# Optimization experiments

Measured on AMD Instinct MI355X. Metric: run time of the kernel, lower is better.

Reference implementation:

```python
import jax, jax.numpy as jnp
import numpy as np

D_MODEL = 1024
N_HEADS = 16
HEAD_DIM = D_MODEL // N_HEADS


def setup_inputs() -> dict:
    key = jax.random.key(0)
    k1, k2, k3 = jax.random.split(key, 3)
    x = jax.random.normal(k1, (8, 1024, D_MODEL), dtype=jnp.float32)
    qkv_w = jax.random.normal(k2, (3 * D_MODEL, D_MODEL), dtype=jnp.float32) * 0.02
    qkv_b = jnp.zeros((3 * D_MODEL,), dtype=jnp.float32)
    proj_w = jax.random.normal(k3, (D_MODEL, D_MODEL), dtype=jnp.float32) * 0.02
    proj_b = jnp.zeros((D_MODEL,), dtype=jnp.float32)
    return {"x": x, "qkv_w": qkv_w, "qkv_b": qkv_b, "proj_w": proj_w, "proj_b": proj_b}


def reference(x, qkv_w, qkv_b, proj_w, proj_b):
    B, N, C = x.shape
    H, Dh = N_HEADS, HEAD_DIM
    # fused QKV projection (torch Linear: x @ W^T + b)
    qkv = x @ qkv_w.T + qkv_b                      # [B, N, 3C]
    qkv = qkv.reshape(B, N, 3, H, Dh).transpose(2, 0, 3, 1, 4)  # [3, B, H, N, Dh]
    q, k, v = qkv[0], qkv[1], qkv[2]
    scale = Dh ** -0.5
    attn = jnp.einsum("bhnd,bhmd->bhnm", q, k) * scale  # [B, H, N, N]
    attn = jax.nn.softmax(attn, axis=-1)
    out = jnp.einsum("bhnm,bhmd->bhnd", attn, v)        # [B, H, N, Dh]
    out = out.transpose(0, 2, 1, 3).reshape(B, N, C)
    return out @ proj_w.T + proj_b
```

## Files before the change

### kernel.cpp

```cpp
#include <hip/hip_runtime.h>
#include <hip/hip_bf16.h>
#include <stdint.h>

#define D_MODEL 1024
#define NHEADS  16
#define HDIM    64
#define SEQ     1024
#define BATCH   8

typedef __bf16 bf16;
typedef bf16  bf16x8 __attribute__((ext_vector_type(8)));
typedef float f32x4  __attribute__((ext_vector_type(4)));
typedef uint32_t u32;

#define VMCNT4   asm volatile("s_waitcnt vmcnt(4)" ::: "memory")
#define VMCNT0   asm volatile("s_waitcnt vmcnt(0)" ::: "memory")
#define LGKMCNT0 asm volatile("s_waitcnt lgkmcnt(0)" ::: "memory")
#define SBAR     __builtin_amdgcn_s_barrier()
#define SCHEDB   __builtin_amdgcn_sched_barrier(0)

__device__ __forceinline__ int swzi(int row, int col) {
    return (row << 6) + (col ^ ((row & 7) << 3));
}

__device__ __forceinline__ void gload_lds16(const bf16* g, bf16* l) {
    __builtin_amdgcn_global_load_lds(
        (const __attribute__((address_space(1))) void*)g,
        (__attribute__((address_space(3))) void*)l, 16, 0, 0);
}

__global__ void cvt3_kernel(const float* __restrict__ x,  bf16* __restrict__ ox, int nx,
                            const float* __restrict__ w1, bf16* __restrict__ o1, int n1,
                            const float* __restrict__ w2, bf16* __restrict__ o2, int n2) {
    int i = (blockIdx.x * 256 + threadIdx.x) * 8;
    const float* src; bf16* dst;
    if (i < nx)           { src = x  + i;            dst = ox + i; }
    else if (i < nx + n1) { src = w1 + (i - nx);     dst = o1 + (i - nx); }
    else if (i < nx + n1 + n2) { src = w2 + (i - nx - n1); dst = o2 + (i - nx - n1); }
    else return;
    float4 a = *reinterpret_cast<const float4*>(src);
    float4 b = *reinterpret_cast<const float4*>(src + 4);
    union { bf16 h[8]; uint4 u; } pk;
    pk.h[0] = (bf16)a.x; pk.h[1] = (bf16)a.y; pk.h[2] = (bf16)a.z; pk.h[3] = (bf16)a.w;
    pk.h[4] = (bf16)b.x; pk.h[5] = (bf16)b.y; pk.h[6] = (bf16)b.z; pk.h[7] = (bf16)b.w;
    *reinterpret_cast<uint4*>(dst) = pk.u;
}

__global__ __launch_bounds__(512, 1)
void qkv_gemm8(const bf16* __restrict__ X, const bf16* __restrict__ W,
               const float* __restrict__ bias,
               bf16* __restrict__ q_ws, bf16* __restrict__ k_ws, bf16* __restrict__ vt_ws)
{
    __shared__ __align__(16) bf16 lds[2][2][2][128 * 64];
    const int K = 1024;
    int bid = blockIdx.x;
    int wg  = (bid & 7) * 48 + (bid >> 3);
    int bm = wg / 12, bn = wg % 12;
    int m0 = bm * 256, n0 = bn * 256;
    int tid = threadIdx.x, lane = tid & 63, wid = tid >> 6;
    int wr = wid >> 2, wc = wid & 3;
    int g = lane >> 4, q = lane & 15;
    int bh_half = wc >> 1;
    int brow0   = (wc & 1) * 64;

    const bf16* srcA[2][2]; const bf16* srcB[2][2]; int dstoff[2];
#pragma unroll
    for (int c = 0; c < 2; ++c) {
        int ch = tid + c * 512;
        int r  = ch >> 3;
        int jg = (ch & 7) ^ (r & 7);
        dstoff[c]  = ch * 8;
        srcA[0][c] = X + (size_t)(m0 + r)       * K + jg * 8;
        srcA[1][c] = X + (size_t)(m0 + 128 + r) * K + jg * 8;
        srcB[0][c] = W + (size_t)(n0 + r)       * K + jg * 8;
        srcB[1][c] = W + (size_t)(n0 + 128 + r) * K + jg * 8;
    }

    f32x4 acc[8][4];
#pragma unroll
    for (int i = 0; i < 8; ++i)
#pragma unroll
        for (int j = 0; j < 4; ++j) acc[i][j] = (f32x4){0.f, 0.f, 0.f, 0.f};

#pragma unroll
    for (int h = 0; h < 2; ++h)
#pragma unroll
        for (int c = 0; c < 2; ++c) { gload_lds16(srcA[h][c], &lds[0][0][h][dstoff[c]]); srcA[h][c] += 64; }
#pragma unroll
    for (int h = 0; h < 2; ++h)
#pragma unroll
        for (int c = 0; c < 2; ++c) { gload_lds16(srcB[h][c], &lds[0][1][h][dstoff[c]]); srcB[h][c] += 64; }

    bf16x8 afr[4][2], bfr[2][2][2];

    for (int t = 0; t < 16; ++t) {
        int p = t & 1, np = p ^ 1;
        bf16* Ah = lds[p][0][wr];
        bf16* Bh = lds[p][1][bh_half];

        if (t < 15) {
#pragma unroll
            for (int h = 0; h < 2; ++h)
#pragma unroll
                for (int c = 0; c < 2; ++c) { gload_lds16(srcA[h][c], &lds[np][0][h][dstoff[c]]); srcA[h][c] += 64; }
            VMCNT4;
        } else {
            VMCNT0;
        }
        SBAR;
#pragma unroll
        for (int m = 0; m < 4; ++m)
#pragma unroll
            for (int kk = 0; kk < 2; ++kk)
                afr[m][kk] = *reinterpret_cast<const bf16x8*>(Ah + swzi(m * 16 + q, kk * 32 + g * 8));
#pragma unroll
        for (int nh = 0; nh < 2; ++nh)
#pragma unroll
            for (int n = 0; n < 2; ++n)
#pragma unroll
                for (int kk = 0; kk < 2; ++kk)
                    bfr[nh][n][kk] = *reinterpret_cast<const bf16x8*>(
                        Bh + swzi(brow0 + (nh * 2 + n) * 16 + q, kk * 32 + g * 8));
        LGKMCNT0; SCHEDB;
        __builtin_amdgcn_s_setprio(1);
#pragma unroll
        for (int m = 0; m < 4; ++m)
#pragma unroll
            for (int n = 0; n < 2; ++n)
#pragma unroll
                for (int kk = 0; kk < 2; ++kk)
                    acc[m][n] = __builtin_amdgcn_mfma_f32_16x16x32_bf16(afr[m][kk], bfr[0][n][kk], acc[m][n], 0, 0, 0);
        __builtin_amdgcn_s_setprio(0);
        SBAR;

        if (t < 15) {
#pragma unroll
            for (int h = 0; h < 2; ++h)
#pragma unroll
                for (int c = 0; c < 2; ++c) { gload_lds16(srcB[h][c], &lds[np][1][h][dstoff[c]]); srcB[h][c] += 64; }
        }
        SCHEDB;
        __builtin_amdgcn_s_setprio(1);
#pragma unroll
        for (int m = 0; m < 4; ++m)
#pragma unroll
            for (int n = 0; n < 2; ++n)
#pragma unroll
                for (int kk = 0; kk < 2; ++kk)
                    acc[m][2 + n] = __builtin_amdgcn_mfma_f32_16x16x32_bf16(afr[m][kk], bfr[1][n][kk], acc[m][2 + n], 0, 0, 0);
        __builtin_amdgcn_s_setprio(0);
        SBAR;

#pragma unroll
        for (int m = 0; m < 4; ++m)
#pragma unroll
            for (int kk = 0; kk < 2; ++kk)
                afr[m][kk] = *reinterpret_cast<const bf16x8*>(Ah + swzi(64 + m * 16 + q, kk * 32 + g * 8));
        LGKMCNT0; SCHEDB;
        __builtin_amdgcn_s_setprio(1);
#pragma unroll
        for (int m = 0; m < 4; ++m)
#pragma unroll
            for (int n = 0; n < 2; ++n)
#pragma unroll
                for (int kk = 0; kk < 2; ++kk)
                    acc[4 + m][n] = __builtin_amdgcn_mfma_f32_16x16x32_bf16(afr[m][kk], bfr[0][n][kk], acc[4 + m][n], 0, 0, 0);
        __builtin_amdgcn_s_setprio(0);
        SBAR;

        SCHEDB;
        __builtin_amdgcn_s_setprio(1);
#pragma unroll
        for (int m = 0; m < 4; ++m)
#pragma unroll
            for (int n = 0; n < 2; ++n)
#pragma unroll
                for (int kk = 0; kk < 2; ++kk)
                    acc[4 + m][2 + n] = __builtin_amdgcn_mfma_f32_16x16x32_bf16(afr[m][kk], bfr[1][n][kk], acc[4 + m][2 + n], 0, 0, 0);
        __builtin_amdgcn_s_setprio(0);
        SBAR;
    }

#pragma unroll
    for (int i = 0; i < 8; ++i) {
        int mbase = m0 + wr * 128 + i * 16 + g * 4;
        int b = mbase >> 10, nrow0 = mbase & 1023;
#pragma unroll
        for (int j = 0; j < 4; ++j) {
            int col = n0 + wc * 64 + j * 16 + q;
            int which = col >> 10, rem = col & 1023;
            int h = rem >> 6, d = rem & 63;
            float bi = bias[col];
            int bh = b * NHEADS + h;
            if (which == 2) {
                union { bf16 h4[4]; uint2 u; } vp;
#pragma unroll
                for (int r = 0; r < 4; ++r) vp.h4[r] = (bf16)(acc[i][j][r] + bi);
                *reinterpret_cast<uint2*>(vt_ws + ((size_t)bh * HDIM + d) * SEQ + nrow0) = vp.u;
            } else {
                bf16* dst = (which == 0) ? q_ws : k_ws;
                float scl = (which == 0) ? 0.125f : 1.0f;
#pragma unroll
                for (int r = 0; r < 4; ++r) {
                    float v = (acc[i][j][r] + bi) * scl;
                    dst[((size_t)bh * SEQ + nrow0 + r) * HDIM + d] = (bf16)v;
                }
            }
        }
    }
}

__device__ __forceinline__ void gemm_tile_acc(
    const bf16* __restrict__ A, const bf16* __restrict__ B, int K,
    int m0, int n0, bf16* As, bf16* Bs,
    f32x4 acc[4][4], int wr, int wc, int lane, int tid)
{
    for (int kt = 0; kt < K; kt += 64) {
        __syncthreads();
#pragma unroll
        for (int c = 0; c < 4; ++c) {
            int chunk = tid + c * 256;
            int r   = chunk >> 3;
            int j   = chunk & 7;
            int jg  = j ^ (r & 7);
            gload_lds16(A + (size_t)(m0 + r) * K + kt + jg * 8, As + chunk * 8);
            gload_lds16(B + (size_t)(n0 + r) * K + kt + jg * 8, Bs + chunk * 8);
        }
        __syncthreads();
#pragma unroll
        for (int kk = 0; kk < 2; ++kk) {
            bf16x8 af[4], bfr[4];
#pragma unroll
            for (int t = 0; t < 4; ++t) {
                af[t]  = *reinterpret_cast<const bf16x8*>(As + swzi(wr * 64 + t * 16 + (lane & 15), kk * 32 + ((lane >> 4) << 3)));
                bfr[t] = *reinterpret_cast<const bf16x8*>(Bs + swzi(wc * 64 + t * 16 + (lane & 15), kk * 32 + ((lane >> 4) << 3)));
            }
#pragma unroll
            for (int i = 0; i < 4; ++i)
#pragma unroll
                for (int j2 = 0; j2 < 4; ++j2)
                    acc[i][j2] = __builtin_amdgcn_mfma_f32_16x16x32_bf16(af[i], bfr[j2], acc[i][j2], 0, 0, 0);
        }
    }
}

__global__ __launch_bounds__(256)
void proj_gemm(const bf16* __restrict__ Ao, const bf16* __restrict__ W,
               const float* __restrict__ bias, float* __restrict__ out)
{
    __shared__ __align__(16) bf16 As[128 * 64];
    __shared__ __align__(16) bf16 Bs[128 * 64];
    const int NB = 1024 / 128;
    int bm = blockIdx.x / NB, bn = blockIdx.x % NB;
    int m0 = bm * 128, n0 = bn * 128;
    int tid = threadIdx.x, lane = tid & 63, w = tid >> 6;
    int wr = w >> 1, wc = w & 1;
    f32x4 acc[4][4];
#pragma unroll
    for (int i = 0; i < 4; ++i)
#pragma unroll
        for (int j = 0; j < 4; ++j) acc[i][j] = (f32x4){0.f, 0.f, 0.f, 0.f};

    gemm_tile_acc(Ao, W, 1024, m0, n0, As, Bs, acc, wr, wc, lane, tid);

#pragma unroll
    for (int i = 0; i < 4; ++i) {
        int mbase = m0 + wr * 64 + i * 16 + ((lane >> 4) << 2);
#pragma unroll
        for (int j = 0; j < 4; ++j) {
            int col = n0 + wc * 64 + j * 16 + (lane & 15);
            float bi = bias[col];
#pragma unroll
            for (int r = 0; r < 4; ++r)
                out[(size_t)(mbase + r) * D_MODEL + col] = acc[i][j][r] + bi;
        }
    }
}

__global__ __launch_bounds__(256)
void attn_kernel(const bf16* __restrict__ Q, const bf16* __restrict__ K,
                 const bf16* __restrict__ Vt, bf16* __restrict__ AO)
{
    __shared__ __align__(16) bf16 kl[128 * 64];
    __shared__ __align__(16) bf16 vl[64 * 128];
    int bh = blockIdx.x & 127;
    int qt = blockIdx.x >> 7;
    int tid = threadIdx.x, lane = tid & 63, w = tid >> 6;
    int g = lane >> 4, q = lane & 15;
    const bf16* Qb  = Q  + (size_t)bh * SEQ * HDIM;
    const bf16* Kb  = K  + (size_t)bh * SEQ * HDIM;
    const bf16* Vtb = Vt + (size_t)bh * HDIM * SEQ;

    int qrow = qt * 64 + w * 16 + q;
    bf16x8 qf[2];
#pragma unroll
    for (int kk = 0; kk < 2; ++kk)
        qf[kk] = *reinterpret_cast<const bf16x8*>(Qb + (size_t)qrow * HDIM + kk * 32 + (g << 3));

    f32x4 o[4];
#pragma unroll
    for (int dt = 0; dt < 4; ++dt) o[dt] = (f32x4){0.f, 0.f, 0.f, 0.f};
    float plsumA = 0.f, plsumB = 0.f;

    const bf16* ksrc[4]; const bf16* vsrc[4]; bf16* kdst[4]; bf16* vdst[4];
#pragma unroll
    for (int c = 0; c < 4; ++c) {
        int ch = tid + c * 256;
        int r  = ch >> 3;
        int j  = ch & 7;
        int jg = j ^ (r & 7);
        int p64  = r & 63;
        int a64  = (((p64 >> 4) & 1) << 5) | (((p64 >> 2) & 3) << 3)
                 | (((p64 >> 5) & 1) << 2) | (p64 & 3);
        int srow = (r & 64) | a64;
        ksrc[c] = Kb + (size_t)srow * HDIM + jg * 8;
        kdst[c] = kl + ch * 8;
        int d   = ch >> 4;
        int jn  = ch & 15;
        int jng = jn ^ (d & 15);
        vsrc[c] = Vtb + (size_t)d * SEQ + jng * 8;
        vdst[c] = vl + ch * 8;
    }

    for (int t = 0; t < 8; ++t) {
        __syncthreads();
#pragma unroll
        for (int c = 0; c < 4; ++c) {
            gload_lds16(ksrc[c], kdst[c]);
            gload_lds16(vsrc[c], vdst[c]);
            ksrc[c] += 128 * HDIM;
            vsrc[c] += 128;
        }
        __syncthreads();

#pragma unroll
        for (int h = 0; h < 2; ++h) {
            f32x4 s[4];
#pragma unroll
            for (int nt = 0; nt < 4; ++nt) {
                s[nt] = (f32x4){0.f, 0.f, 0.f, 0.f};
#pragma unroll
                for (int kk = 0; kk < 2; ++kk) {
                    bf16x8 kf = *reinterpret_cast<const bf16x8*>(
                        kl + swzi(h * 64 + nt * 16 + q, kk * 32 + (g << 3)));
                    s[nt] = __builtin_amdgcn_mfma_f32_16x16x32_bf16(kf, qf[kk], s[nt], 0, 0, 0);
                }
            }

            u32 pkk[4][2];
#pragma unroll
            for (int nt = 0; nt < 4; ++nt)
#pragma unroll
                for (int half = 0; half < 2; ++half) {
                    float pa = __expf(s[nt][2 * half]     - 4.0f);
                    float pb = __expf(s[nt][2 * half + 1] - 4.0f);
                    if (half == 0) plsumA += pa + pb; else plsumB += pa + pb;
                    union { bf16 hh[2]; u32 u; } pw;
                    pw.hh[0] = (bf16)pa; pw.hh[1] = (bf16)pb;
                    pkk[nt][half] = pw.u;
                }

#pragma unroll
            for (int ks = 0; ks < 2; ++ks) {
                union { u32 u[4]; bf16x8 v; } pb;
                pb.u[0] = pkk[ks][0];
                pb.u[1] = pkk[ks][1];
                pb.u[2] = pkk[2 + ks][0];
                pb.u[3] = pkk[2 + ks][1];
#pragma unroll
                for (int dt = 0; dt < 4; ++dt) {
                    int d = dt * 16 + q;
                    int ch = (8 * h + 4 * ks + g) ^ q;
                    bf16x8 vfr = *reinterpret_cast<const bf16x8*>(vl + d * 128 + ch * 8);
                    o[dt] = __builtin_amdgcn_mfma_f32_16x16x32_bf16(vfr, pb.v, o[dt], 0, 0, 0);
                }
            }
        }
    }

    float plsum = plsumA + plsumB;
    plsum += __shfl_xor(plsum, 16);
    plsum += __shfl_xor(plsum, 32);
    float inv = 1.f / plsum;

    int b = bh >> 4, h = bh & 15;
    size_t base = ((size_t)b * SEQ + qrow) * D_MODEL + h * HDIM;
#pragma unroll
    for (int dt = 0; dt < 4; ++dt) {
        union { bf16 h4[4]; uint2 u; } ob;
#pragma unroll
        for (int r = 0; r < 4; ++r) ob.h4[r] = (bf16)(o[dt][r] * inv);
        *reinterpret_cast<uint2*>(AO + base + dt * 16 + (g << 2)) = ob.u;
    }
}

extern "C" void kernel_launch(void* const* d_in, const int* in_sizes, int n_in,
                              void* d_out, int out_size, void* d_ws, size_t ws_size,
                              hipStream_t stream) {
    const float* x      = (const float*)d_in[0];
    const float* qkv_w  = (const float*)d_in[1];
    const float* qkv_b  = (const float*)d_in[2];
    const float* proj_w = (const float*)d_in[3];
    const float* proj_b = (const float*)d_in[4];
    float* out = (float*)d_out;
    char* ws = (char*)d_ws;

    bf16* x_bf    = (bf16*)(ws);
    bf16* wqkv_bf = (bf16*)(ws + (size_t)(16 << 20));
    bf16* wproj_bf= (bf16*)(ws + (size_t)(22 << 20));
    bf16* q_ws    = (bf16*)(ws + (size_t)(24 << 20));
    bf16* k_ws    = (bf16*)(ws + (size_t)(40 << 20));
    bf16* vt_ws   = (bf16*)(ws + (size_t)(56 << 20));
    bf16* ao_ws   = x_bf;

    const int NX = 8192 * 1024, N1 = 3072 * 1024, N2 = 1024 * 1024;
    cvt3_kernel<<<(NX + N1 + N2) / 2048, 256, 0, stream>>>(
        x, x_bf, NX, qkv_w, wqkv_bf, N1, proj_w, wproj_bf, N2);

    qkv_gemm8<<<384, 512, 0, stream>>>(x_bf, wqkv_bf, qkv_b, q_ws, k_ws, vt_ws);
    attn_kernel<<<128 * 16, 256, 0, stream>>>(q_ws, k_ws, vt_ws, ao_ws);
    proj_gemm<<<64 * 8, 256, 0, stream>>>(ao_ws, wproj_bf, proj_b, out);
}
```

Measured before the change: 158.7 us.

## Retile QKV GEMM to 256x192 tiles and double attention block size

The QKV GEMM moves from 256x256 tiles on 384 blocks to 256x192 tiles on 512 blocks. Each wave now computes a 128x48 sub-tile, which removes two of the four MFMA phases per k-step, and the B tile is loaded as three 64-row slabs. The attention kernel goes from 256 to 512 threads with 128 query rows per block, so each K/V tile loaded into LDS is shared by twice as many query rows and half as many blocks are launched. This trades per-block arithmetic intensity in the GEMM for better CU fill (512 blocks on 256 CUs), and in attention trades fewer loads per query row against lower occupancy granularity.

```diff
diff --git a/kernel.cpp b/kernel.cpp
--- a/kernel.cpp
+++ b/kernel.cpp
@@ -51,58 +51,61 @@
                const float* __restrict__ bias,
                bf16* __restrict__ q_ws, bf16* __restrict__ k_ws, bf16* __restrict__ vt_ws)
 {
-    __shared__ __align__(16) bf16 lds[2][2][2][128 * 64];
+    __shared__ __align__(16) bf16 lds_a[2][2][128 * 64];
+    __shared__ __align__(16) bf16 lds_b[2][192 * 64];
     const int K = 1024;
     int bid = blockIdx.x;
-    int wg  = (bid & 7) * 48 + (bid >> 3);
-    int bm = wg / 12, bn = wg % 12;
-    int m0 = bm * 256, n0 = bn * 256;
+    int wg  = (bid & 7) * 64 + (bid >> 3);
+    int bm = wg >> 4, bn = wg & 15;
+    int m0 = bm * 256, n0 = bn * 192;
     int tid = threadIdx.x, lane = tid & 63, wid = tid >> 6;
     int wr = wid >> 2, wc = wid & 3;
     int g = lane >> 4, q = lane & 15;
-    int bh_half = wc >> 1;
-    int brow0   = (wc & 1) * 64;
-
-    const bf16* srcA[2][2]; const bf16* srcB[2][2]; int dstoff[2];
+
+    const bf16* srcA[2][2]; const bf16* srcB[3]; int dstA[2]; int dstB;
 #pragma unroll
     for (int c = 0; c < 2; ++c) {
         int ch = tid + c * 512;
         int r  = ch >> 3;
         int jg = (ch & 7) ^ (r & 7);
-        dstoff[c]  = ch * 8;
+        dstA[c]    = ch * 8;
         srcA[0][c] = X + (size_t)(m0 + r)       * K + jg * 8;
         srcA[1][c] = X + (size_t)(m0 + 128 + r) * K + jg * 8;
-        srcB[0][c] = W + (size_t)(n0 + r)       * K + jg * 8;
-        srcB[1][c] = W + (size_t)(n0 + 128 + r) * K + jg * 8;
-    }
-
-    f32x4 acc[8][4];
+    }
+    {
+        int r  = tid >> 3;
+        int jg = (tid & 7) ^ (r & 7);
+        dstB    = tid * 8;
+        srcB[0] = W + (size_t)(n0 + r)       * K + jg * 8;
+        srcB[1] = W + (size_t)(n0 + 64 + r)  * K + jg * 8;
+        srcB[2] = W + (size_t)(n0 + 128 + r) * K + jg * 8;
+    }
+
+    f32x4 acc[8][3];
 #pragma unroll
     for (int i = 0; i < 8; ++i)
 #pragma unroll
-        for (int j = 0; j < 4; ++j) acc[i][j] = (f32x4){0.f, 0.f, 0.f, 0.f};
+        for (int j = 0; j < 3; ++j) acc[i][j] = (f32x4){0.f, 0.f, 0.f, 0.f};
 
 #pragma unroll
     for (int h = 0; h < 2; ++h)
 #pragma unroll
-        for (int c = 0; c < 2; ++c) { gload_lds16(srcA[h][c], &lds[0][0][h][dstoff[c]]); srcA[h][c] += 64; }
-#pragma unroll
-    for (int h = 0; h < 2; ++h)
-#pragma unroll
-        for (int c = 0; c < 2; ++c) { gload_lds16(srcB[h][c], &lds[0][1][h][dstoff[c]]); srcB[h][c] += 64; }
-
-    bf16x8 afr[4][2], bfr[2][2][2];
+        for (int c = 0; c < 2; ++c) { gload_lds16(srcA[h][c], &lds_a[0][h][dstA[c]]); srcA[h][c] += 64; }
+#pragma unroll
+    for (int tt = 0; tt < 3; ++tt) { gload_lds16(srcB[tt], &lds_b[0][tt * 4096 + dstB]); srcB[tt] += 64; }
+
+    bf16x8 afr[4][2], bfr[3][2];
 
     for (int t = 0; t < 16; ++t) {
         int p = t & 1, np = p ^ 1;
-        bf16* Ah = lds[p][0][wr];
-        bf16* Bh = lds[p][1][bh_half];
+        bf16* Ah = lds_a[p][wr];
+        bf16* Bt = lds_b[p];
 
         if (t < 15) {
 #pragma unroll
             for (int h = 0; h < 2; ++h)
 #pragma unroll
-                for (int c = 0; c < 2; ++c) { gload_lds16(srcA[h][c], &lds[np][0][h][dstoff[c]]); srcA[h][c] += 64; }
+                for (int c = 0; c < 2; ++c) { gload_lds16(srcA[h][c], &lds_a[np][h][dstA[c]]); srcA[h][c] += 64; }
             VMCNT4;
         } else {
             VMCNT0;
@@ -114,43 +117,26 @@
             for (int kk = 0; kk < 2; ++kk)
                 afr[m][kk] = *reinterpret_cast<const bf16x8*>(Ah + swzi(m * 16 + q, kk * 32 + g * 8));
 #pragma unroll
-        for (int nh = 0; nh < 2; ++nh)
-#pragma unroll
-            for (int n = 0; n < 2; ++n)
-#pragma unroll
-                for (int kk = 0; kk < 2; ++kk)
-                    bfr[nh][n][kk] = *reinterpret_cast<const bf16x8*>(
-                        Bh + swzi(brow0 + (nh * 2 + n) * 16 + q, kk * 32 + g * 8));
+        for (int j = 0; j < 3; ++j)
+#pragma unroll
+            for (int kk = 0; kk < 2; ++kk)
+                bfr[j][kk] = *reinterpret_cast<const bf16x8*>(Bt + swzi(wc * 48 + j * 16 + q, kk * 32 + g * 8));
         LGKMCNT0; SCHEDB;
         __builtin_amdgcn_s_setprio(1);
 #pragma unroll
         for (int m = 0; m < 4; ++m)
 #pragma unroll
-            for (int n = 0; n < 2; ++n)
+            for (int j = 0; j < 3; ++j)
 #pragma unroll
                 for (int kk = 0; kk < 2; ++kk)
-                    acc[m][n] = __builtin_amdgcn_mfma_f32_16x16x32_bf16(afr[m][kk], bfr[0][n][kk], acc[m][n], 0, 0, 0);
+                    acc[m][j] = __builtin_amdgcn_mfma_f32_16x16x32_bf16(afr[m][kk], bfr[j][kk], acc[m][j], 0, 0, 0);
         __builtin_amdgcn_s_setprio(0);
         SBAR;
 
         if (t < 15) {
 #pragma unroll
-            for (int h = 0; h < 2; ++h)
-#pragma unroll
-                for (int c = 0; c < 2; ++c) { gload_lds16(srcB[h][c], &lds[np][1][h][dstoff[c]]); srcB[h][c] += 64; }
-        }
-        SCHEDB;
-        __builtin_amdgcn_s_setprio(1);
-#pragma unroll
-        for (int m = 0; m < 4; ++m)
-#pragma unroll
-            for (int n = 0; n < 2; ++n)
-#pragma unroll
-                for (int kk = 0; kk < 2; ++kk)
-                    acc[m][2 + n] = __builtin_amdgcn_mfma_f32_16x16x32_bf16(afr[m][kk], bfr[1][n][kk], acc[m][2 + n], 0, 0, 0);
-        __builtin_amdgcn_s_setprio(0);
-        SBAR;
-
+            for (int tt = 0; tt < 3; ++tt) { gload_lds16(srcB[tt], &lds_b[np][tt * 4096 + dstB]); srcB[tt] += 64; }
+        }
 #pragma unroll
         for (int m = 0; m < 4; ++m)
 #pragma unroll
@@ -161,33 +147,21 @@
 #pragma unroll
         for (int m = 0; m < 4; ++m)
 #pragma unroll
-            for (int n = 0; n < 2; ++n)
+            for (int j = 0; j < 3; ++j)
 #pragma unroll
                 for (int kk = 0; kk < 2; ++kk)
-                    acc[4 + m][n] = __builtin_amdgcn_mfma_f32_16x16x32_bf16(afr[m][kk], bfr[0][n][kk], acc[4 + m][n], 0, 0, 0);
+                    acc[4 + m][j] = __builtin_amdgcn_mfma_f32_16x16x32_bf16(afr[m][kk], bfr[j][kk], acc[4 + m][j], 0, 0, 0);
         __builtin_amdgcn_s_setprio(0);
         SBAR;
-
-        SCHEDB;
-        __builtin_amdgcn_s_setprio(1);
-#pragma unroll
-        for (int m = 0; m < 4; ++m)
-#pragma unroll
-            for (int n = 0; n < 2; ++n)
-#pragma unroll
-                for (int kk = 0; kk < 2; ++kk)
-                    acc[4 + m][2 + n] = __builtin_amdgcn_mfma_f32_16x16x32_bf16(afr[m][kk], bfr[1][n][kk], acc[4 + m][2 + n], 0, 0, 0);
-        __builtin_amdgcn_s_setprio(0);
-        SBAR;
     }
 
 #pragma unroll
     for (int i = 0; i < 8; ++i) {
-        int mbase = m0 + wr * 128 + i * 16 + g * 4;
+        int mbase = m0 + wr * 128 + (i >> 2) * 64 + (i & 3) * 16 + g * 4;
         int b = mbase >> 10, nrow0 = mbase & 1023;
 #pragma unroll
-        for (int j = 0; j < 4; ++j) {
-            int col = n0 + wc * 64 + j * 16 + q;
+        for (int j = 0; j < 3; ++j) {
+            int col = n0 + wc * 48 + j * 16 + q;
             int which = col >> 10, rem = col & 1023;
             int h = rem >> 6, d = rem & 63;
             float bi = bias[col];
@@ -277,7 +251,7 @@
     }
 }
 
-__global__ __launch_bounds__(256)
+__global__ __launch_bounds__(512)
 void attn_kernel(const bf16* __restrict__ Q, const bf16* __restrict__ K,
                  const bf16* __restrict__ Vt, bf16* __restrict__ AO)
 {
@@ -291,7 +265,7 @@
     const bf16* Kb  = K  + (size_t)bh * SEQ * HDIM;
     const bf16* Vtb = Vt + (size_t)bh * HDIM * SEQ;
 
-    int qrow = qt * 64 + w * 16 + q;
+    int qrow = qt * 128 + w * 16 + q;
     bf16x8 qf[2];
 #pragma unroll
     for (int kk = 0; kk < 2; ++kk)
@@ -302,10 +276,10 @@
     for (int dt = 0; dt < 4; ++dt) o[dt] = (f32x4){0.f, 0.f, 0.f, 0.f};
     float plsumA = 0.f, plsumB = 0.f;
 
-    const bf16* ksrc[4]; const bf16* vsrc[4]; bf16* kdst[4]; bf16* vdst[4];
-#pragma unroll
-    for (int c = 0; c < 4; ++c) {
-        int ch = tid + c * 256;
+    const bf16* ksrc[2]; const bf16* vsrc[2]; bf16* kdst[2]; bf16* vdst[2];
+#pragma unroll
+    for (int c = 0; c < 2; ++c) {
+        int ch = tid + c * 512;
         int r  = ch >> 3;
         int j  = ch & 7;
         int jg = j ^ (r & 7);
@@ -325,7 +299,7 @@
     for (int t = 0; t < 8; ++t) {
         __syncthreads();
 #pragma unroll
-        for (int c = 0; c < 4; ++c) {
+        for (int c = 0; c < 2; ++c) {
             gload_lds16(ksrc[c], kdst[c]);
             gload_lds16(vsrc[c], vdst[c]);
             ksrc[c] += 128 * HDIM;
@@ -417,7 +391,7 @@
     cvt3_kernel<<<(NX + N1 + N2) / 2048, 256, 0, stream>>>(
         x, x_bf, NX, qkv_w, wqkv_bf, N1, proj_w, wproj_bf, N2);
 
-    qkv_gemm8<<<384, 512, 0, stream>>>(x_bf, wqkv_bf, qkv_b, q_ws, k_ws, vt_ws);
-    attn_kernel<<<128 * 16, 256, 0, stream>>>(q_ws, k_ws, vt_ws, ao_ws);
+    qkv_gemm8<<<512, 512, 0, stream>>>(x_bf, wqkv_bf, qkv_b, q_ws, k_ws, vt_ws);
+    attn_kernel<<<1024, 512, 0, stream>>>(q_ws, k_ws, vt_ws, ao_ws);
     proj_gemm<<<64 * 8, 256, 0, stream>>>(ao_ws, wproj_bf, proj_b, out);
 }
```

New measurement: 164.3 us. 1.04x slower.
